# Kernel optimization log

Hardware: AMD Instinct MI355X
Metric: run time of the kernel (lower is better)

Reference implementation:

```python
import jax, jax.numpy as jnp
import numpy as np

B, T, E, H = 2, 4096, 1024, 16
D = E // H  # head dim = 64

def setup_inputs() -> dict:
    key = jax.random.key(0)
    ks = jax.random.split(key, 5)
    x = jax.random.normal(ks[0], (B, T, E), dtype=jnp.float32)
    # torch Linear(n_embed, 3*n_embed): y = x @ W.T + b ; we store W already transposed as (E, 3E)
    w_qkv = jax.random.normal(ks[1], (E, 3 * E), dtype=jnp.float32) * (1.0 / np.sqrt(E))
    b_qkv = jax.random.normal(ks[2], (3 * E,), dtype=jnp.float32) * 0.02
    w_out = jax.random.normal(ks[3], (E, E), dtype=jnp.float32) * (1.0 / np.sqrt(E))
    b_out = jax.random.normal(ks[4], (E,), dtype=jnp.float32) * 0.02
    return {"x": x, "w_qkv": w_qkv, "b_qkv": b_qkv, "w_out": w_out, "b_out": b_out}

def reference(x, w_qkv, b_qkv, w_out, b_out):
    b, t, e = x.shape
    qkv = x @ w_qkv + b_qkv                      # (B,T,3E)
    # matches torch: view(B,T,H,3D) then chunk(3, dim=-1)
    qkv = qkv.reshape(b, t, H, 3 * D)
    q, k, v = jnp.split(qkv, 3, axis=-1)          # each (B,T,H,D)
    q = q.transpose(0, 2, 1, 3)                   # (B,H,T,D)
    k = k.transpose(0, 2, 1, 3)
    v = v.transpose(0, 2, 1, 3)
    scores = jnp.einsum('bhqd,bhkd->bhqk', q, k) / jnp.sqrt(jnp.float32(D))
    causal = jnp.tril(jnp.ones((t, t), dtype=bool))
    scores = jnp.where(causal, scores, jnp.float32(-jnp.inf))
    w = jax.nn.softmax(scores, axis=-1)           # (B,H,T,T)
    out = jnp.einsum('bhqk,bhkd->bhqd', w, v)     # (B,H,T,D)
    out = out.transpose(0, 2, 1, 3).reshape(b, t, e)
    return out @ w_out + b_out
```

## Files before the change

### kernel.cpp

```cpp
#include <hip/hip_runtime.h>
#include <stdint.h>
#include <math.h>

#define T_SEQ 4096

typedef __attribute__((ext_vector_type(8))) short short8;
typedef __attribute__((ext_vector_type(4))) float f32x4;
typedef __attribute__((ext_vector_type(4))) uint16_t u16x4;

__device__ __forceinline__ uint16_t f2bf(float f) {
  uint32_t u = __float_as_uint(f);
  u += 0x7FFFu + ((u >> 16) & 1u);
  return (uint16_t)(u >> 16);
}

__device__ __forceinline__ void gload_lds16(const uint16_t* g, uint16_t* l) {
  __builtin_amdgcn_global_load_lds(
      (const __attribute__((address_space(1))) void*)g,
      (__attribute__((address_space(3))) void*)l, 16, 0, 0);
}

__global__ void __launch_bounds__(256) k_cvt(const float* __restrict__ in,
                                             uint16_t* __restrict__ out, int n4) {
  int i = blockIdx.x * 256 + threadIdx.x;
  if (i >= n4) return;
  float4 v = reinterpret_cast<const float4*>(in)[i];
  u16x4 o = { f2bf(v.x), f2bf(v.y), f2bf(v.z), f2bf(v.w) };
  reinterpret_cast<u16x4*>(out)[i] = o;
}

__global__ void __launch_bounds__(256) k_tc(const float* __restrict__ w,
                                            uint16_t* __restrict__ wt, int R, int C) {
  __shared__ uint16_t tile[32][33];
  int tx = threadIdx.x & 31, ty = threadIdx.x >> 5;
  int r0 = blockIdx.y * 32, c0 = blockIdx.x * 32;
#pragma unroll
  for (int i = 0; i < 4; i++)
    tile[ty + 8 * i][tx] = f2bf(w[(size_t)(r0 + ty + 8 * i) * C + c0 + tx]);
  __syncthreads();
#pragma unroll
  for (int i = 0; i < 4; i++)
    wt[(size_t)(c0 + ty + 8 * i) * R + r0 + tx] = tile[tx][ty + 8 * i];
}

__global__ void __launch_bounds__(256) k_vt(const uint16_t* __restrict__ qkv,
                                            uint16_t* __restrict__ vT) {
  __shared__ uint16_t tile[64][65];
  const int bh = blockIdx.y, b = bh >> 4, h = bh & 15;
  const int t0 = blockIdx.x * 64;
  const int tid = threadIdx.x;
  const int r = tid >> 3, c8 = tid & 7;
  const uint16_t* src = qkv + ((size_t)b * T_SEQ + t0) * 3072 + h * 192 + 128;
#pragma unroll
  for (int i = 0; i < 2; i++) {
    int row = r + 32 * i;
    short8 v = *reinterpret_cast<const short8*>(src + (size_t)row * 3072 + c8 * 8);
#pragma unroll
    for (int j = 0; j < 8; j++) tile[row][c8 * 8 + j] = (uint16_t)v[j];
  }
  __syncthreads();
  uint16_t* dst = vT + ((size_t)bh * 64) * T_SEQ + t0;
#pragma unroll
  for (int i = 0; i < 2; i++) {
    int d = r + 32 * i;
    short8 v;
#pragma unroll
    for (int j = 0; j < 8; j++) v[j] = (short)tile[c8 * 8 + j][d];
    *reinterpret_cast<short8*>(dst + (size_t)d * T_SEQ + c8 * 8) = v;
  }
}

template <int BF16_OUT>
__global__ void __launch_bounds__(256) k_gemm(const uint16_t* __restrict__ A,
                                              const uint16_t* __restrict__ BT,
                                              const float* __restrict__ bias,
                                              void* __restrict__ Cout,
                                              int M, int N, int K) {
  __shared__ __align__(16) uint16_t As[128][32];
  __shared__ __align__(16) uint16_t Bs[128][32];
  const int tid = threadIdx.x;
  const int lane = tid & 63, wid = tid >> 6;
  const int lr = lane & 15, lg = lane >> 4;
  const int wr = wid >> 1, wc = wid & 1;

  const int bid = blockIdx.x;
  const int cpx = gridDim.x >> 3;
  const int lin = (bid & 7) * cpx + (bid >> 3);
  const int nxt = N >> 7;
  const int m0 = (lin / nxt) * 128, n0 = (lin % nxt) * 128;

  const f32x4 vzero = {0.f, 0.f, 0.f, 0.f};
  f32x4 acc[4][4];
#pragma unroll
  for (int i = 0; i < 4; i++)
#pragma unroll
    for (int j = 0; j < 4; j++) acc[i][j] = vzero;

  const int seg0 = wid * 2;
  const int srow = lane >> 2;
  const int scol = (lane & 3) * 8;
  const uint16_t* Ag = A + (size_t)m0 * K;
  const uint16_t* Bg = BT + (size_t)n0 * K;
  const size_t ra0 = (size_t)(seg0 * 16 + srow) * K + scol;
  const size_t ra1 = (size_t)(seg0 * 16 + 16 + srow) * K + scol;

  for (int kk = 0; kk < K; kk += 32) {
    __syncthreads();
    gload_lds16(Ag + ra0 + kk, &As[seg0 * 16][0]);
    gload_lds16(Ag + ra1 + kk, &As[seg0 * 16 + 16][0]);
    gload_lds16(Bg + ra0 + kk, &Bs[seg0 * 16][0]);
    gload_lds16(Bg + ra1 + kk, &Bs[seg0 * 16 + 16][0]);
    __syncthreads();
    short8 af[4], bfr[4];
#pragma unroll
    for (int mi = 0; mi < 4; mi++)
      af[mi] = *reinterpret_cast<const short8*>(&As[wr * 64 + mi * 16 + lr][lg * 8]);
#pragma unroll
    for (int nj = 0; nj < 4; nj++)
      bfr[nj] = *reinterpret_cast<const short8*>(&Bs[wc * 64 + nj * 16 + lr][lg * 8]);
#pragma unroll
    for (int mi = 0; mi < 4; mi++)
#pragma unroll
      for (int nj = 0; nj < 4; nj++)
        acc[mi][nj] = __builtin_amdgcn_mfma_f32_16x16x32_bf16(af[mi], bfr[nj], acc[mi][nj], 0, 0, 0);
  }

#pragma unroll
  for (int nj = 0; nj < 4; nj++) {
    int col = n0 + wc * 64 + nj * 16 + lr;
    float bv = bias[col];
#pragma unroll
    for (int mi = 0; mi < 4; mi++) {
      int rowb = m0 + wr * 64 + mi * 16 + lg * 4;
#pragma unroll
      for (int r = 0; r < 4; r++) {
        float v = acc[mi][nj][r] + bv;
        if (BF16_OUT)
          ((uint16_t*)Cout)[(size_t)(rowb + r) * N + col] = f2bf(v);
        else
          ((float*)Cout)[(size_t)(rowb + r) * N + col] = v;
      }
    }
  }
}

#define KVB 64
__global__ void __launch_bounds__(256) k_attn(const uint16_t* __restrict__ qkv,
                                              const uint16_t* __restrict__ vT,
                                              uint16_t* __restrict__ out) {
  __shared__ __align__(16) char lds[40960];
  const int tid = threadIdx.x;
  const int lane = tid & 63, wid = tid >> 6;
  const int lr = lane & 15, lg = lane >> 4;
  char* psb = lds + 32768 + wid * 2048;

  const int bid = blockIdx.x;
  const int xcd = bid & 7, j = bid >> 3;
  const int bh = xcd * 4 + (j & 3);
  const int qt = 31 - (j >> 2);
  const int b = bh >> 4, h = bh & 15;
  const int q0 = qt * 128;
  const size_t rowbase = (size_t)b * T_SEQ;
  const int hoff = h * 192;
  const uint16_t* Kg = qkv + rowbase * 3072 + hoff + 64;
  const uint16_t* Vg = vT + (size_t)bh * 64 * T_SEQ;

  const int sr = tid >> 3, sc = tid & 7;
  const int wsw = (sc ^ (sr & 7)) * 16;
  const int swz = (lr & 7) << 4;
  const float C_SC = 0.180336881f;

  short8 ones8;
#pragma unroll
  for (int i = 0; i < 8; i++) ones8[i] = (lr == 0) ? (short)0x3F80 : (short)0;

  const f32x4 vzero = {0.f, 0.f, 0.f, 0.f};

  short8 qf[2][2];
#pragma unroll
  for (int qq = 0; qq < 2; qq++)
#pragma unroll
    for (int c = 0; c < 2; c++) {
      short8 raw = *reinterpret_cast<const short8*>(
          qkv + (rowbase + q0 + wid * 32 + qq * 16 + lr) * 3072 + hoff + c * 32 + lg * 8);
      union { short8 s; uint32_t u[4]; } pk;
#pragma unroll
      for (int e = 0; e < 4; e++) {
        float f0 = __uint_as_float(((uint32_t)(uint16_t)raw[2 * e]) << 16) * C_SC;
        float f1 = __uint_as_float(((uint32_t)(uint16_t)raw[2 * e + 1]) << 16) * C_SC;
        asm("v_cvt_pk_bf16_f32 %0, %1, %2" : "=v"(pk.u[e]) : "v"(f0), "v"(f1));
      }
      qf[qq][c] = pk.s;
    }

  f32x4 o[2][4];
  f32x4 o4[2];
#pragma unroll
  for (int qq = 0; qq < 2; qq++) {
    o4[qq] = vzero;
#pragma unroll
    for (int dt = 0; dt < 4; dt++) o[qq][dt] = vzero;
  }

  const int nkt = 2 * qt + 2;
  const int qwmax = q0 + wid * 32 + 31;

  short8 rk0, rk1, rv0, rv1;
  rk0 = *reinterpret_cast<const short8*>(Kg + (size_t)sr * 3072 + sc * 8);
  rk1 = *reinterpret_cast<const short8*>(Kg + (size_t)(sr + 32) * 3072 + sc * 8);
  rv0 = *reinterpret_cast<const short8*>(Vg + (size_t)sr * T_SEQ + sc * 8);
  rv1 = *reinterpret_cast<const short8*>(Vg + (size_t)(sr + 32) * T_SEQ + sc * 8);
  {
    char* kb0 = lds;
    char* vb0 = lds + 16384;
    *reinterpret_cast<short8*>(kb0 + sr * 128 + wsw) = rk0;
    *reinterpret_cast<short8*>(kb0 + (sr + 32) * 128 + wsw) = rk1;
    *reinterpret_cast<short8*>(vb0 + sr * 128 + wsw) = rv0;
    *reinterpret_cast<short8*>(vb0 + (sr + 32) * 128 + wsw) = rv1;
  }
  if (nkt > 1) {
    rk0 = *reinterpret_cast<const short8*>(Kg + (size_t)(KVB + sr) * 3072 + sc * 8);
    rk1 = *reinterpret_cast<const short8*>(Kg + (size_t)(KVB + sr + 32) * 3072 + sc * 8);
    rv0 = *reinterpret_cast<const short8*>(Vg + (size_t)sr * T_SEQ + KVB + sc * 8);
    rv1 = *reinterpret_cast<const short8*>(Vg + (size_t)(sr + 32) * T_SEQ + KVB + sc * 8);
  }

  for (int kt = 0; kt < nkt; kt++) {
    __syncthreads();
    if (kt + 1 < nkt) {
      const int nsel = (kt + 1) & 1;
      char* kb = lds + (nsel ? 8192 : 0);
      char* vb = lds + 16384 + (nsel ? 8192 : 0);
      *reinterpret_cast<short8*>(kb + sr * 128 + wsw) = rk0;
      *reinterpret_cast<short8*>(kb + (sr + 32) * 128 + wsw) = rk1;
      *reinterpret_cast<short8*>(vb + sr * 128 + wsw) = rv0;
      *reinterpret_cast<short8*>(vb + (sr + 32) * 128 + wsw) = rv1;
      if (kt + 2 < nkt) {
        int k0n = (kt + 2) * KVB;
        rk0 = *reinterpret_cast<const short8*>(Kg + (size_t)(k0n + sr) * 3072 + sc * 8);
        rk1 = *reinterpret_cast<const short8*>(Kg + (size_t)(k0n + sr + 32) * 3072 + sc * 8);
        rv0 = *reinterpret_cast<const short8*>(Vg + (size_t)sr * T_SEQ + k0n + sc * 8);
        rv1 = *reinterpret_cast<const short8*>(Vg + (size_t)(sr + 32) * T_SEQ + k0n + sc * 8);
      }
    }

    if (kt * KVB <= qwmax) {
      const int csel = kt & 1;
      char* kcur = lds + (csel ? 8192 : 0);
      char* vcur = lds + 16384 + (csel ? 8192 : 0);
      f32x4 s0[4], s1[4];
      __builtin_amdgcn_s_setprio(1);
#pragma unroll
      for (int t = 0; t < 4; t++) {
        int row = t * 16 + lr;
        short8 kf0 = *reinterpret_cast<const short8*>(
            kcur + row * 128 + ((lg * 16) ^ swz));
        short8 kf1 = *reinterpret_cast<const short8*>(
            kcur + row * 128 + ((64 + lg * 16) ^ swz));
        s0[t] = __builtin_amdgcn_mfma_f32_16x16x32_bf16(kf0, qf[0][0], vzero, 0, 0, 0);
        s0[t] = __builtin_amdgcn_mfma_f32_16x16x32_bf16(kf1, qf[0][1], s0[t], 0, 0, 0);
        s1[t] = __builtin_amdgcn_mfma_f32_16x16x32_bf16(kf0, qf[1][0], vzero, 0, 0, 0);
        s1[t] = __builtin_amdgcn_mfma_f32_16x16x32_bf16(kf1, qf[1][1], s1[t], 0, 0, 0);
      }
      __builtin_amdgcn_s_setprio(0);
      short8 vf[4][2];
#pragma unroll
      for (int dt = 0; dt < 4; dt++)
#pragma unroll
        for (int c2 = 0; c2 < 2; c2++)
          vf[dt][c2] = *reinterpret_cast<const short8*>(
              vcur + (dt * 16 + lr) * 128 + ((c2 * 64 + lg * 16) ^ swz));

#pragma unroll
      for (int qq = 0; qq < 2; qq++) {
        f32x4* s = qq ? s1 : s0;
        const int qrow = q0 + wid * 32 + qq * 16 + lr;
        const bool notfull = (kt * KVB + 63 > q0 + wid * 32 + qq * 16);
#pragma unroll
        for (int t = 0; t < 4; t++)
#pragma unroll
          for (int r = 0; r < 4; r++) {
            float v = s[t][r];
            if (notfull) {
              int key = kt * KVB + t * 16 + lg * 4 + r;
              if (key > qrow) v = -INFINITY;
            }
            s[t][r] = __builtin_amdgcn_exp2f(v);
          }
#pragma unroll
        for (int t = 0; t < 4; t++) {
          uint32_t w0, w1;
          asm("v_cvt_pk_bf16_f32 %0, %1, %2" : "=v"(w0) : "v"(s[t][0]), "v"(s[t][1]));
          asm("v_cvt_pk_bf16_f32 %0, %1, %2" : "=v"(w1) : "v"(s[t][2]), "v"(s[t][3]));
          uint2 ww; ww.x = w0; ww.y = w1;
          *reinterpret_cast<uint2*>(psb + lr * 128 + ((t * 32 + lg * 8) ^ swz)) = ww;
        }
        __builtin_amdgcn_s_setprio(1);
#pragma unroll
        for (int c2 = 0; c2 < 2; c2++) {
          short8 pf = *reinterpret_cast<const short8*>(
              psb + lr * 128 + ((c2 * 64 + lg * 16) ^ swz));
          o4[qq] = __builtin_amdgcn_mfma_f32_16x16x32_bf16(ones8, pf, o4[qq], 0, 0, 0);
#pragma unroll
          for (int dt = 0; dt < 4; dt++)
            o[qq][dt] = __builtin_amdgcn_mfma_f32_16x16x32_bf16(vf[dt][c2], pf, o[qq][dt], 0, 0, 0);
        }
        __builtin_amdgcn_s_setprio(0);
      }
    }
  }

  __syncthreads();
  char* scrb = lds + wid * 4096;
#pragma unroll
  for (int qq = 0; qq < 2; qq++) {
    float lsum = __shfl(o4[qq][0], lr);
    float inv = 1.0f / lsum;
#pragma unroll
    for (int dt = 0; dt < 4; dt++)
#pragma unroll
      for (int r = 0; r < 4; r++)
        *reinterpret_cast<float*>(scrb + lr * 256 + ((dt * 64 + lg * 16) ^ swz) + r * 4) =
            o[qq][dt][r] * inv;
    int row = lane >> 2, ch = lane & 3;
    uint16_t tmp[16];
#pragma unroll
    for (int k = 0; k < 4; k++) {
      f32x4 vv = *reinterpret_cast<const f32x4*>(
          scrb + row * 256 + ((ch * 64 + k * 16) ^ ((row & 7) << 4)));
#pragma unroll
      for (int j2 = 0; j2 < 4; j2++) tmp[k * 4 + j2] = f2bf(vv[j2]);
    }
    uint16_t* op = out + (rowbase + q0 + wid * 32 + qq * 16 + row) * 1024 + h * 64 + ch * 16;
    *reinterpret_cast<short8*>(op) = *reinterpret_cast<const short8*>(tmp);
    *reinterpret_cast<short8*>(op + 8) = *reinterpret_cast<const short8*>(tmp + 8);
  }
}

extern "C" void kernel_launch(void* const* d_in, const int* in_sizes, int n_in,
                              void* d_out, int out_size, void* d_ws, size_t ws_size,
                              hipStream_t stream) {
  const float* x = (const float*)d_in[0];
  const float* w_qkv = (const float*)d_in[1];
  const float* b_qkv = (const float*)d_in[2];
  const float* w_out = (const float*)d_in[3];
  const float* b_out = (const float*)d_in[4];
  float* out = (float*)d_out;

  uint8_t* ws = (uint8_t*)d_ws;
  uint16_t* x_bf  = (uint16_t*)(ws);
  uint16_t* wqkvT = (uint16_t*)(ws + (16u << 20));
  uint16_t* woutT = (uint16_t*)(ws + (22u << 20));
  uint16_t* qkv   = (uint16_t*)(ws + (24u << 20));
  uint16_t* vTbuf = (uint16_t*)(ws + (72u << 20));
  uint16_t* attn_o = x_bf;

  k_cvt<<<8192, 256, 0, stream>>>(x, x_bf, 2097152);
  k_tc<<<dim3(96, 32), 256, 0, stream>>>(w_qkv, wqkvT, 1024, 3072);
  k_tc<<<dim3(32, 32), 256, 0, stream>>>(w_out, woutT, 1024, 1024);
  k_gemm<1><<<1536, 256, 0, stream>>>(x_bf, wqkvT, b_qkv, qkv, 8192, 3072, 1024);
  k_vt<<<dim3(64, 32), 256, 0, stream>>>(qkv, vTbuf);
  k_attn<<<1024, 256, 0, stream>>>(qkv, vTbuf, attn_o);
  k_gemm<0><<<512, 256, 0, stream>>>(attn_o, woutT, b_out, out, 8192, 1024, 1024);
}
```

Baseline: 251.7 us.

## Double-buffer GEMM LDS tiles with BK=64, XOR swizzle and MFMA priority

The projection GEMM kernel now uses two LDS buffers with a K-tile of 64. The tile for step t+2 is prefetched with direct global-to-LDS loads while step t is computed, which removes one of the two barriers per K step. LDS columns are XOR-swizzled to reduce bank conflicts, and MFMA sections are wrapped in s_setprio. Tile rasterization is changed to M-major order and launch bounds request 2 blocks per CU. The cost is double the LDS footprint and more register pressure.

```diff
diff --git a/kernel.cpp b/kernel.cpp
--- a/kernel.cpp
+++ b/kernel.cpp
@@ -71,13 +71,13 @@
 }
 
 template <int BF16_OUT>
-__global__ void __launch_bounds__(256) k_gemm(const uint16_t* __restrict__ A,
-                                              const uint16_t* __restrict__ BT,
-                                              const float* __restrict__ bias,
-                                              void* __restrict__ Cout,
-                                              int M, int N, int K) {
-  __shared__ __align__(16) uint16_t As[128][32];
-  __shared__ __align__(16) uint16_t Bs[128][32];
+__global__ void __launch_bounds__(256, 2) k_gemm(const uint16_t* __restrict__ A,
+                                                 const uint16_t* __restrict__ BT,
+                                                 const float* __restrict__ bias,
+                                                 void* __restrict__ Cout,
+                                                 int M, int N, int K) {
+  __shared__ __align__(16) uint16_t As[2][128 * 64];
+  __shared__ __align__(16) uint16_t Bs[2][128 * 64];
   const int tid = threadIdx.x;
   const int lane = tid & 63, wid = tid >> 6;
   const int lr = lane & 15, lg = lane >> 4;
@@ -86,8 +86,9 @@
   const int bid = blockIdx.x;
   const int cpx = gridDim.x >> 3;
   const int lin = (bid & 7) * cpx + (bid >> 3);
-  const int nxt = N >> 7;
-  const int m0 = (lin / nxt) * 128, n0 = (lin % nxt) * 128;
+  const int mt = M >> 7;
+  const int n0 = (lin / mt) * 128;
+  const int m0 = (lin % mt) * 128;
 
   const f32x4 vzero = {0.f, 0.f, 0.f, 0.f};
   f32x4 acc[4][4];
@@ -96,34 +97,57 @@
 #pragma unroll
     for (int j = 0; j < 4; j++) acc[i][j] = vzero;
 
-  const int seg0 = wid * 2;
-  const int srow = lane >> 2;
-  const int scol = (lane & 3) * 8;
-  const uint16_t* Ag = A + (size_t)m0 * K;
-  const uint16_t* Bg = BT + (size_t)n0 * K;
-  const size_t ra0 = (size_t)(seg0 * 16 + srow) * K + scol;
-  const size_t ra1 = (size_t)(seg0 * 16 + 16 + srow) * K + scol;
-
-  for (int kk = 0; kk < K; kk += 32) {
+  const int sl = lane >> 3, ss = lane & 7;
+  const int swzs = (ss ^ sl) * 8;
+  const uint16_t* a0 = A + (size_t)(m0 + wid * 32 + sl) * K + swzs;
+  const uint16_t* b0 = BT + (size_t)(n0 + wid * 32 + sl) * K + swzs;
+  const size_t r8 = (size_t)8 * K;
+
+#define STAGE(bsel, t)                                                   \
+  do {                                                                   \
+    const int koff_ = (t) * 64;                                          \
+    gload_lds16(a0 + koff_,          &As[bsel][(wid * 32 + 0) * 64]);    \
+    gload_lds16(a0 + r8 + koff_,     &As[bsel][(wid * 32 + 8) * 64]);    \
+    gload_lds16(a0 + 2 * r8 + koff_, &As[bsel][(wid * 32 + 16) * 64]);   \
+    gload_lds16(a0 + 3 * r8 + koff_, &As[bsel][(wid * 32 + 24) * 64]);   \
+    gload_lds16(b0 + koff_,          &Bs[bsel][(wid * 32 + 0) * 64]);    \
+    gload_lds16(b0 + r8 + koff_,     &Bs[bsel][(wid * 32 + 8) * 64]);    \
+    gload_lds16(b0 + 2 * r8 + koff_, &Bs[bsel][(wid * 32 + 16) * 64]);   \
+    gload_lds16(b0 + 3 * r8 + koff_, &Bs[bsel][(wid * 32 + 24) * 64]);   \
+  } while (0)
+
+  const int nt = K >> 6;
+  const int fsw = lr & 7;
+  STAGE(0, 0);
+  STAGE(1, 1);
+  __syncthreads();
+
+  for (int t = 0; t < nt; ++t) {
+    const int cur = t & 1;
+#pragma unroll
+    for (int ks = 0; ks < 2; ++ks) {
+      const int col = (((ks * 4 + lg) ^ fsw) * 8);
+      short8 af[4], bf[4];
+#pragma unroll
+      for (int mi = 0; mi < 4; ++mi)
+        af[mi] = *reinterpret_cast<const short8*>(
+            &As[cur][(wr * 64 + mi * 16 + lr) * 64 + col]);
+#pragma unroll
+      for (int nj = 0; nj < 4; ++nj)
+        bf[nj] = *reinterpret_cast<const short8*>(
+            &Bs[cur][(wc * 64 + nj * 16 + lr) * 64 + col]);
+      __builtin_amdgcn_s_setprio(1);
+#pragma unroll
+      for (int mi = 0; mi < 4; ++mi)
+#pragma unroll
+        for (int nj = 0; nj < 4; ++nj)
+          acc[mi][nj] = __builtin_amdgcn_mfma_f32_16x16x32_bf16(af[mi], bf[nj], acc[mi][nj], 0, 0, 0);
+      __builtin_amdgcn_s_setprio(0);
+    }
     __syncthreads();
-    gload_lds16(Ag + ra0 + kk, &As[seg0 * 16][0]);
-    gload_lds16(Ag + ra1 + kk, &As[seg0 * 16 + 16][0]);
-    gload_lds16(Bg + ra0 + kk, &Bs[seg0 * 16][0]);
-    gload_lds16(Bg + ra1 + kk, &Bs[seg0 * 16 + 16][0]);
-    __syncthreads();
-    short8 af[4], bfr[4];
-#pragma unroll
-    for (int mi = 0; mi < 4; mi++)
-      af[mi] = *reinterpret_cast<const short8*>(&As[wr * 64 + mi * 16 + lr][lg * 8]);
-#pragma unroll
-    for (int nj = 0; nj < 4; nj++)
-      bfr[nj] = *reinterpret_cast<const short8*>(&Bs[wc * 64 + nj * 16 + lr][lg * 8]);
-#pragma unroll
-    for (int mi = 0; mi < 4; mi++)
-#pragma unroll
-      for (int nj = 0; nj < 4; nj++)
-        acc[mi][nj] = __builtin_amdgcn_mfma_f32_16x16x32_bf16(af[mi], bfr[nj], acc[mi][nj], 0, 0, 0);
-  }
+    if (t + 2 < nt) STAGE(cur, t + 2);
+  }
+#undef STAGE
 
 #pragma unroll
   for (int nj = 0; nj < 4; nj++) {
```

New measurement: 248.6 us. About the same (-1.2%).
